# Kernel optimization log

Measured on AMD Instinct MI355X. Metric: run time of the kernel, lower is better.

Reference implementation:

```python
import jax, jax.numpy as jnp
import numpy as np

M, K, N = 32, 8192, 8192      # tokens, infeatures, outfeatures
GROUP = 128                   # quantization group size along K
PACK = 8                      # 32 bits / 4 bits per value


def _dequant(qweight, scales):
    """Unpack int4 nibbles (packed 8-per-int32 along K) and apply per-group
    symmetric dequant: w = (q - 8) * scale, matching Marlin's fused dequant."""
    kp, n = qweight.shape  # (K//8, N)
    shifts = (4 * jnp.arange(PACK, dtype=jnp.int32))[None, :, None]
    q = ((qweight[:, None, :] >> shifts) & 15)          # (K//8, 8, N)
    q = q.reshape(kp * PACK, n).astype(jnp.float32)     # (K, N)
    groups = scales.shape[0]
    gsz = (kp * PACK) // groups
    w = (q.reshape(groups, gsz, n) - 8.0) * scales[:, None, :]
    return w.reshape(kp * PACK, n)                      # (K, N) fp


def setup_inputs() -> dict:
    key = jax.random.key(0)
    kA, kQ, kS, kB = jax.random.split(key, 4)
    A = jax.random.normal(kA, (M, K), jnp.float32)
    # draw raw 4-bit codes then pack 8 of them into each int32 along K
    q4 = jax.random.randint(kQ, (K, N), 0, 16, jnp.int32)
    shifts = (4 * jnp.arange(PACK, dtype=jnp.int32))[None, :, None]
    qweight = jnp.sum(q4.reshape(K // PACK, PACK, N) << shifts, axis=1).astype(jnp.int32)
    scales = jax.random.uniform(kS, (K // GROUP, N), jnp.float32, 0.005, 0.02)
    bias = jax.random.normal(kB, (N,), jnp.float32) * 0.01
    return {"A": A, "qweight": qweight, "scales": scales, "bias": bias}


def reference(A, qweight, scales, bias):
    # Marlin mul(A, B, C, s) computes C = A @ dequant(B, s); then + bias
    W = _dequant(qweight, scales)          # (K, N)
    return A @ W + bias                    # (M, N)
```

## Files before the change

### kernel.cpp

```cpp
#include <hip/hip_runtime.h>
#include <hip/hip_bf16.h>
#include <stdint.h>

#define M_DIM 32
#define K_DIM 8192
#define N_DIM 8192
#define NGROUPS 64
#define GSZ 128
#define KSPLIT 2
#define KHALF (K_DIM / KSPLIT)
#define GHALF (NGROUPS / KSPLIT)
#define BN 64

typedef __attribute__((ext_vector_type(8))) short short8;
typedef __attribute__((ext_vector_type(4))) float floatx4;

__global__ void marlin_prep_kernel(const float* __restrict__ A,
                                   uint16_t* __restrict__ Abf,
                                   float* __restrict__ R) {
    const int m = blockIdx.x;
    const int qtr = blockIdx.y;
    const int t = threadIdx.x;
    const int octet = qtr * 256 + t;
    const int k0 = octet * 8;

    const float* a = A + m * K_DIM + k0;
    uint16_t b[8];
    float sum = 0.f;
#pragma unroll
    for (int j = 0; j < 8; j++) {
        union { __hip_bfloat16 h; uint16_t u; } cv;
        cv.h = __float2bfloat16(a[j]);
        b[j] = cv.u;
        sum += __bfloat162float(cv.h);
    }
    uint32_t w0 = (uint32_t)b[0] | ((uint32_t)b[4] << 16);
    uint32_t w1 = (uint32_t)b[1] | ((uint32_t)b[5] << 16);
    uint32_t w2 = (uint32_t)b[2] | ((uint32_t)b[6] << 16);
    uint32_t w3 = (uint32_t)b[3] | ((uint32_t)b[7] << 16);
    uint4 packed = make_uint4(w0, w1, w2, w3);
    *(uint4*)(Abf + (size_t)m * K_DIM + k0) = packed;

#pragma unroll
    for (int off = 1; off < 16; off <<= 1) sum += __shfl_xor(sum, off, 16);
    if ((t & 15) == 0) R[m * NGROUPS + qtr * 16 + (t >> 4)] = sum;
}

__global__ __launch_bounds__(512) void
MarlinQuantLinear_68556267979256_kernel(const int* __restrict__ qw,
                                        const float* __restrict__ scales,
                                        const float* __restrict__ bias,
                                        const uint16_t* __restrict__ Abf,
                                        const float* __restrict__ R,
                                        float* __restrict__ out) {
    __shared__ __align__(16) uint16_t a_lds[32 * 136];
    __shared__ float r_lds[32 * 33];

    const int bx = blockIdx.x;
    const int bz = blockIdx.y;
    const int nbase = bx * BN;
    const int kbase = bz * KHALF;
    const int gbase = bz * GHALF;

    const int tid = threadIdx.x;
    const int w = tid >> 6;
    const int lane = tid & 63;
    const int quad = lane >> 4;
    const int l16 = lane & 15;
    const int mtile = w & 1;
    const int ntile = w >> 1;
    const int ncol = nbase + ntile * 16 + l16;

    {
        int i = tid;
#pragma unroll
        for (int rep = 0; rep < 2; rep++, i += 512) {
            int mm = i >> 5, gg = i & 31;
            r_lds[mm * 33 + gg] = R[mm * NGROUPS + gbase + gg];
        }
    }

    const int lm = tid >> 4;
    const int lseg = tid & 15;
    const uint4* Asrc = (const uint4*)Abf;
    const int abase = lm * (K_DIM / 8) + (kbase >> 3) + lseg;

    const int kp_base = kbase >> 3;
    floatx4 C = {0.f, 0.f, 0.f, 0.f};

    for (int g = 0; g < GHALF; g++) {
        __syncthreads();
        {
            uint4 av = Asrc[abase + g * 16];
            *(uint4*)&a_lds[lm * 136 + lseg * 8] = av;
        }
        __syncthreads();

        const float s = scales[(gbase + g) * N_DIM + ncol];
        floatx4 accg = {0.f, 0.f, 0.f, 0.f};
#pragma unroll
        for (int t = 0; t < 4; t++) {
            const uint32_t q =
                (uint32_t)qw[(kp_base + g * 16 + t * 4 + quad) * N_DIM + ncol];
            union { uint32_t u[4]; short8 v; } fb;
            fb.u[0] = ( q        & 0x000F000Fu) | 0x43004300u;
            fb.u[1] = ((q >> 4)  & 0x000F000Fu) | 0x43004300u;
            fb.u[2] = ((q >> 8)  & 0x000F000Fu) | 0x43004300u;
            fb.u[3] = ((q >> 12) & 0x000F000Fu) | 0x43004300u;
            const short8 fa =
                *(const short8*)&a_lds[(mtile * 16 + l16) * 136 + t * 32 + quad * 8];
            accg = __builtin_amdgcn_mfma_f32_16x16x32_bf16(fa, fb.v, accg, 0, 0, 0);
        }
#pragma unroll
        for (int r = 0; r < 4; r++) {
            const float Rv = r_lds[(mtile * 16 + quad * 4 + r) * 33 + g];
            const float tval = fmaf(-136.0f, Rv, accg[r]);
            C[r] = fmaf(s, tval, C[r]);
        }
    }

    const float bv = (bz == 0) ? bias[ncol] : 0.0f;
#pragma unroll
    for (int r = 0; r < 4; r++) {
        const int m = mtile * 16 + quad * 4 + r;
        atomicAdd(&out[(size_t)m * N_DIM + ncol], C[r] + bv);
    }
}

extern "C" void kernel_launch(void* const* d_in, const int* in_sizes, int n_in,
                              void* d_out, int out_size, void* d_ws, size_t ws_size,
                              hipStream_t stream) {
    const float* A      = (const float*)d_in[0];
    const int*   qw     = (const int*)d_in[1];
    const float* scales = (const float*)d_in[2];
    const float* bias   = (const float*)d_in[3];
    float* out = (float*)d_out;

    uint16_t* Abf = (uint16_t*)d_ws;
    float*    R   = (float*)((char*)d_ws + (size_t)M_DIM * K_DIM * 2);

    hipMemsetAsync(d_out, 0, (size_t)M_DIM * N_DIM * sizeof(float), stream);
    marlin_prep_kernel<<<dim3(M_DIM, 4), 256, 0, stream>>>(A, Abf, R);
    MarlinQuantLinear_68556267979256_kernel<<<dim3(N_DIM / BN, KSPLIT), 512, 0, stream>>>(
        qw, scales, bias, Abf, R, out);
}
```

Measured before the change: 105.7 us.

## Split K four ways, read A directly from global, fold output zeroing into prep

Raises the K split from 2 to 4 so the grid has twice as many blocks and more parallelism for the memory-bound int4 weight stream. The LDS staging of A and its per-group barriers are removed; each lane now loads its bf16 A fragment straight from global (L2-resident). The output memset is folded into the prep kernel, removing one launch, and the 136*R correction is precomputed in LDS. In exchange it doubles the atomic adds to the output and adds redundant global A reads across blocks.

```diff
diff --git a/kernel.cpp b/kernel.cpp
--- a/kernel.cpp
+++ b/kernel.cpp
@@ -7,9 +7,9 @@
 #define N_DIM 8192
 #define NGROUPS 64
 #define GSZ 128
-#define KSPLIT 2
-#define KHALF (K_DIM / KSPLIT)
-#define GHALF (NGROUPS / KSPLIT)
+#define KSPLIT 4
+#define KPART (K_DIM / KSPLIT)
+#define GPART (NGROUPS / KSPLIT)
 #define BN 64
 
 typedef __attribute__((ext_vector_type(8))) short short8;
@@ -17,12 +17,20 @@
 
 __global__ void marlin_prep_kernel(const float* __restrict__ A,
                                    uint16_t* __restrict__ Abf,
-                                   float* __restrict__ R) {
+                                   float* __restrict__ R,
+                                   float4* __restrict__ out4) {
     const int m = blockIdx.x;
     const int qtr = blockIdx.y;
     const int t = threadIdx.x;
     const int octet = qtr * 256 + t;
     const int k0 = octet * 8;
+
+    {
+        const int gtid = (qtr * 32 + m) * 256 + t;
+        const float4 z = make_float4(0.f, 0.f, 0.f, 0.f);
+        out4[gtid * 2] = z;
+        out4[gtid * 2 + 1] = z;
+    }
 
     const float* a = A + m * K_DIM + k0;
     uint16_t b[8];
@@ -46,21 +54,20 @@
     if ((t & 15) == 0) R[m * NGROUPS + qtr * 16 + (t >> 4)] = sum;
 }
 
-__global__ __launch_bounds__(512) void
+__global__ __launch_bounds__(512, 4) void
 MarlinQuantLinear_68556267979256_kernel(const int* __restrict__ qw,
                                         const float* __restrict__ scales,
                                         const float* __restrict__ bias,
                                         const uint16_t* __restrict__ Abf,
                                         const float* __restrict__ R,
                                         float* __restrict__ out) {
-    __shared__ __align__(16) uint16_t a_lds[32 * 136];
-    __shared__ float r_lds[32 * 33];
+    __shared__ float r_lds[32 * 17];
 
     const int bx = blockIdx.x;
     const int bz = blockIdx.y;
     const int nbase = bx * BN;
-    const int kbase = bz * KHALF;
-    const int gbase = bz * GHALF;
+    const int kbase = bz * KPART;
+    const int gbase = bz * GPART;
 
     const int tid = threadIdx.x;
     const int w = tid >> 6;
@@ -72,49 +79,36 @@
     const int ncol = nbase + ntile * 16 + l16;
 
     {
-        int i = tid;
-#pragma unroll
-        for (int rep = 0; rep < 2; rep++, i += 512) {
-            int mm = i >> 5, gg = i & 31;
-            r_lds[mm * 33 + gg] = R[mm * NGROUPS + gbase + gg];
-        }
+        const int mm = tid >> 4, gg = tid & 15;
+        r_lds[mm * 17 + gg] = 136.0f * R[mm * NGROUPS + gbase + gg];
     }
+    __syncthreads();
 
-    const int lm = tid >> 4;
-    const int lseg = tid & 15;
-    const uint4* Asrc = (const uint4*)Abf;
-    const int abase = lm * (K_DIM / 8) + (kbase >> 3) + lseg;
+    const uint16_t* arow = Abf + (size_t)(mtile * 16 + l16) * K_DIM
+                               + kbase + quad * 8;
+    const int* qcol = qw + (size_t)(kbase >> 3) * N_DIM + ncol;
+    const float* scol = scales + (size_t)gbase * N_DIM + ncol;
 
-    const int kp_base = kbase >> 3;
     floatx4 C = {0.f, 0.f, 0.f, 0.f};
 
-    for (int g = 0; g < GHALF; g++) {
-        __syncthreads();
-        {
-            uint4 av = Asrc[abase + g * 16];
-            *(uint4*)&a_lds[lm * 136 + lseg * 8] = av;
-        }
-        __syncthreads();
-
-        const float s = scales[(gbase + g) * N_DIM + ncol];
+#pragma unroll 2
+    for (int g = 0; g < GPART; g++) {
+        const float s = scol[g * N_DIM];
         floatx4 accg = {0.f, 0.f, 0.f, 0.f};
 #pragma unroll
         for (int t = 0; t < 4; t++) {
-            const uint32_t q =
-                (uint32_t)qw[(kp_base + g * 16 + t * 4 + quad) * N_DIM + ncol];
+            const uint32_t q = (uint32_t)qcol[(g * 16 + t * 4 + quad) * N_DIM];
             union { uint32_t u[4]; short8 v; } fb;
             fb.u[0] = ( q        & 0x000F000Fu) | 0x43004300u;
             fb.u[1] = ((q >> 4)  & 0x000F000Fu) | 0x43004300u;
             fb.u[2] = ((q >> 8)  & 0x000F000Fu) | 0x43004300u;
             fb.u[3] = ((q >> 12) & 0x000F000Fu) | 0x43004300u;
-            const short8 fa =
-                *(const short8*)&a_lds[(mtile * 16 + l16) * 136 + t * 32 + quad * 8];
+            const short8 fa = *(const short8*)(arow + g * 128 + t * 32);
             accg = __builtin_amdgcn_mfma_f32_16x16x32_bf16(fa, fb.v, accg, 0, 0, 0);
         }
 #pragma unroll
         for (int r = 0; r < 4; r++) {
-            const float Rv = r_lds[(mtile * 16 + quad * 4 + r) * 33 + g];
-            const float tval = fmaf(-136.0f, Rv, accg[r]);
+            const float tval = accg[r] - r_lds[(mtile * 16 + quad * 4 + r) * 17 + g];
             C[r] = fmaf(s, tval, C[r]);
         }
     }
@@ -139,8 +133,7 @@
     uint16_t* Abf = (uint16_t*)d_ws;
     float*    R   = (float*)((char*)d_ws + (size_t)M_DIM * K_DIM * 2);
 
-    hipMemsetAsync(d_out, 0, (size_t)M_DIM * N_DIM * sizeof(float), stream);
-    marlin_prep_kernel<<<dim3(M_DIM, 4), 256, 0, stream>>>(A, Abf, R);
+    marlin_prep_kernel<<<dim3(M_DIM, 4), 256, 0, stream>>>(A, Abf, R, (float4*)out);
     MarlinQuantLinear_68556267979256_kernel<<<dim3(N_DIM / BN, KSPLIT), 512, 0, stream>>>(
         qw, scales, bias, Abf, R, out);
 }
```

After: 112.3 us. 1.06x slower.
